# Optimization experiments

Hardware: AMD Instinct MI355X
Metric: run time of the kernel (lower is better)

## Reference

```python
import jax, jax.numpy as jnp
import numpy as np

B, N_PIC, C, H, W, P = 32, 4, 3, 224, 224, 16
HP = H // P  # 14
NP = HP * HP  # 196 patches
D = C * P * P  # 768 = hidden_size


def setup_inputs() -> dict:
    key = jax.random.key(0)
    ks = jax.random.split(key, 12)
    s = 0.02
    def lin(k, din, dout):
        kw, kb = jax.random.split(k)
        return (jax.random.normal(kw, (din, dout), jnp.float32) * s,
                jax.random.normal(kb, (dout,), jnp.float32) * s)
    W1, b1 = lin(ks[0], D, D)
    Wq, bq = lin(ks[1], D, D)
    Wk, bk = lin(ks[2], D, D)
    Wv, bv = lin(ks[3], D, D)
    Wo1, bo1 = lin(ks[4], D, D)
    Wo2, bo2 = lin(ks[5], D, D)
    x = jax.random.normal(ks[6], (B, N_PIC, C, H, W), jnp.float32)
    return {"x": x, "W1": W1, "b1": b1, "Wq": Wq, "bq": bq, "Wk": Wk,
            "bk": bk, "Wv": Wv, "bv": bv, "Wo1": Wo1, "bo1": bo1,
            "Wo2": Wo2, "bo2": bo2}


def reference(x, W1, b1, Wq, bq, Wk, bk, Wv, bv, Wo1, bo1, Wo2, bo2):
    b = x.shape[0]
    # patchify: matches torch unfold(3,P,P).unfold(4,P,P) + permute + view
    # -> [b, N, num_patches, C*P*P] with (C, ph, pw) ordering in last dim
    p = x.reshape(b, N_PIC, C, HP, P, HP, P)
    p = p.transpose(0, 1, 3, 5, 2, 4, 6).reshape(b, N_PIC, NP, D)
    h = p @ W1 + b1  # [b, N, S, D]
    # attention: query always from picture 0; key/value per picture (batched)
    Q = h[:, 0] @ Wq + bq          # [b, S, D]
    K = h @ Wk + bk                # [b, N, S, D]
    V = h @ Wv + bv                # [b, N, S, D]
    scale = 1.0 / jnp.sqrt(jnp.float32(D))
    scores = jnp.einsum('bsd,bnmd->bnsm', Q, K) * scale  # [b, N, S, S]
    attn = jax.nn.softmax(scores, axis=-1)
    wv = jnp.einsum('bnsm,bnmd->bnsd', attn, V)           # [b, N, S, D]
    out = jax.nn.relu(wv @ Wo1 + bo1) @ Wo2 + bo2
    return out
```

## Files before the change

kernel.cpp:

```cpp
#include <hip/hip_runtime.h>

typedef __bf16 bf16;
typedef __bf16 bf16x8 __attribute__((ext_vector_type(8)));
typedef float  f32x4  __attribute__((ext_vector_type(4)));


__global__ __launch_bounds__(256) void patchify_k(const float* __restrict__ x,
                                                  bf16* __restrict__ p) {
  int t = blockIdx.x * 256 + threadIdx.x;
  if (t >= 128 * 3 * 14 * 16 * 14) return;
  int j  = t % 14; t /= 14;
  int ph = t % 16; t /= 16;
  int i  = t % 14; t /= 14;
  int c  = t % 3;  t /= 3;
  int bn = t;
  const float* src = x + (((long long)(bn * 3 + c) * 224 + (i * 16 + ph)) * 224 + j * 16);
  bf16* dst = p + ((long long)(bn * 196 + (i * 14 + j)) * 768 + c * 256 + ph * 16);
  bf16 tmp[16];
  for (int k = 0; k < 16; k += 4) {
    float4 f = *(const float4*)(src + k);
    tmp[k + 0] = (bf16)f.x; tmp[k + 1] = (bf16)f.y;
    tmp[k + 2] = (bf16)f.z; tmp[k + 3] = (bf16)f.w;
  }
  *(bf16x8*)(dst)     = *(bf16x8*)&tmp[0];
  *(bf16x8*)(dst + 8) = *(bf16x8*)&tmp[8];
}

__global__ __launch_bounds__(256) void wtrans_k(const float* __restrict__ w0,
                                                const float* __restrict__ w1,
                                                const float* __restrict__ w2,
                                                const float* __restrict__ w3,
                                                const float* __restrict__ w4,
                                                const float* __restrict__ w5,
                                                bf16* __restrict__ out) {
  __shared__ float tile[32][33];
  const float* W;
  switch (blockIdx.z) {
    case 0: W = w0; break; case 1: W = w1; break; case 2: W = w2; break;
    case 3: W = w3; break; case 4: W = w4; break; default: W = w5; break;
  }
  bf16* o = out + (long long)blockIdx.z * 768 * 768;
  int nb = blockIdx.x * 32, kb = blockIdx.y * 32;
  int c = threadIdx.x & 31, r = threadIdx.x >> 5;
  for (int rr = 0; rr < 32; rr += 8)
    tile[r + rr][c] = W[(long long)(kb + r + rr) * 768 + nb + c];
  __syncthreads();
  for (int rr = 0; rr < 32; rr += 8)
    o[(long long)(nb + r + rr) * 768 + kb + c] = (bf16)tile[c][r + rr];
}

__global__ __launch_bounds__(256) void vtrans_k(const bf16* __restrict__ V,
                                                bf16* __restrict__ Vt) {
  __shared__ short tile[32][33];
  int z = blockIdx.z;
  const short* v = (const short*)(V + (long long)z * 196 * 768);
  short* vt = (short*)(Vt + (long long)z * 768 * 224);
  int db = blockIdx.x * 32;
  int mb = blockIdx.y * 32;
  int c = threadIdx.x & 31, r = threadIdx.x >> 5;
  for (int rr = 0; rr < 32; rr += 8) {
    int m = mb + r + rr;
    short val = 0;
    if (m < 196) val = v[(long long)m * 768 + db + c];
    tile[r + rr][c] = val;
  }
  __syncthreads();
  for (int rr = 0; rr < 32; rr += 8) {
    int d = db + r + rr;
    vt[(long long)d * 224 + mb + c] = tile[c][r + rr];
  }
}

__global__ __launch_bounds__(64) void softmax_k(const float* __restrict__ S,
                                                bf16* __restrict__ attn) {
  const int row = blockIdx.x;
  const float* sr = S + (long long)row * 196;
  const int l = threadIdx.x;
  float v0 = sr[l];
  float v1 = sr[l + 64];
  float v2 = sr[l + 128];
  float v3 = (l + 192 < 196) ? sr[l + 192] : -1e30f;
  float mx = fmaxf(fmaxf(v0, v1), fmaxf(v2, v3));
  for (int o = 32; o > 0; o >>= 1) mx = fmaxf(mx, __shfl_xor(mx, o));
  float e0 = __expf(v0 - mx);
  float e1 = __expf(v1 - mx);
  float e2 = __expf(v2 - mx);
  float e3 = (l + 192 < 196) ? __expf(v3 - mx) : 0.f;
  float s = e0 + e1 + e2 + e3;
  for (int o = 32; o > 0; o >>= 1) s += __shfl_xor(s, o);
  float inv = 1.0f / s;
  bf16* ar = attn + (long long)row * 224;
  ar[l]       = (bf16)(e0 * inv);
  ar[l + 64]  = (bf16)(e1 * inv);
  ar[l + 128] = (bf16)(e2 * inv);
  int m3 = l + 192;
  if (m3 < 196) ar[m3] = (bf16)(e3 * inv);
  else if (m3 < 224) ar[m3] = (bf16)0.0f;
}

__device__ __forceinline__ void gld16(const bf16* g, bf16* l) {
  __builtin_amdgcn_global_load_lds(
      (const __attribute__((address_space(1))) unsigned int*)g,
      (__attribute__((address_space(3))) unsigned int*)l, 16, 0, 0);
}

__global__ __launch_bounds__(256) void gemm128(
    const bf16* __restrict__ A, const bf16* __restrict__ Bt,
    const float* __restrict__ bias, void* __restrict__ Cout,
    int M, int N, int K, int gr, long long gs,
    long long strideAz, int a_zdiv, long long strideBz, long long strideCz,
    float scale, int relu, int out_bf16) {
  __shared__ __align__(16) bf16 As[128 * 32];
  __shared__ __align__(16) bf16 Bs[128 * 32];

  const int tid = threadIdx.x;
  const int lane = tid & 63;
  const int w = tid >> 6;
  const int wm = w & 1, wn = w >> 1;
  const int z = blockIdx.z;
  const int n0 = blockIdx.x * 128, m0 = blockIdx.y * 128;

  const bf16* Az  = A  + (long long)(z / a_zdiv) * strideAz;
  const bf16* Btz = Bt + (long long)z * strideBz;

  const int r0 = tid >> 2, kc0 = (tid & 3) * 8;
  int ar0 = m0 + r0;       if (ar0 >= M) ar0 = M - 1;
  int ar1 = m0 + 64 + r0;  if (ar1 >= M) ar1 = M - 1;
  const long long aoff0 = (long long)(ar0 / gr) * gs + (long long)(ar0 % gr) * K + kc0;
  const long long aoff1 = (long long)(ar1 / gr) * gs + (long long)(ar1 % gr) * K + kc0;
  int br0 = n0 + r0;       if (br0 >= N) br0 = N - 1;
  int br1 = n0 + 64 + r0;  if (br1 >= N) br1 = N - 1;
  const long long boff0 = (long long)br0 * K + kc0;
  const long long boff1 = (long long)br1 * K + kc0;

  bf16* asD0 = As + (long long)w * 512;
  bf16* asD1 = As + 2048 + (long long)w * 512;
  bf16* bsD0 = Bs + (long long)w * 512;
  bf16* bsD1 = Bs + 2048 + (long long)w * 512;

  f32x4 acc[4][4] = {};
  const int fr = lane & 15, fq = lane >> 4;

  for (int ko = 0; ko < K; ko += 32) {
    __syncthreads();
    gld16(Az + aoff0 + ko, asD0);
    gld16(Az + aoff1 + ko, asD1);
    gld16(Btz + boff0 + ko, bsD0);
    gld16(Btz + boff1 + ko, bsD1);
    __syncthreads();

    bf16x8 a[4], b[4];
#pragma unroll
    for (int mi = 0; mi < 4; mi++)
      a[mi] = *(const bf16x8*)&As[(wm * 64 + mi * 16 + fr) * 32 + fq * 8];
#pragma unroll
    for (int ni = 0; ni < 4; ni++)
      b[ni] = *(const bf16x8*)&Bs[(wn * 64 + ni * 16 + fr) * 32 + fq * 8];
#pragma unroll
    for (int mi = 0; mi < 4; mi++)
#pragma unroll
      for (int ni = 0; ni < 4; ni++)
        acc[mi][ni] = __builtin_amdgcn_mfma_f32_16x16x32_bf16(a[mi], b[ni], acc[mi][ni], 0, 0, 0);
  }

  const long long cz = (long long)z * strideCz;
#pragma unroll
  for (int ni = 0; ni < 4; ni++) {
    int col = n0 + wn * 64 + ni * 16 + fr;
    if (col >= N) continue;
    float bb = bias ? bias[col] : 0.f;
#pragma unroll
    for (int mi = 0; mi < 4; mi++) {
      int rbase = m0 + wm * 64 + mi * 16 + fq * 4;
#pragma unroll
      for (int r = 0; r < 4; r++) {
        int row = rbase + r;
        if (row >= M) continue;
        float v = acc[mi][ni][r] * scale + bb;
        if (relu) v = fmaxf(v, 0.f);
        long long idx = cz + (long long)row * N + col;
        if (out_bf16) ((bf16*)Cout)[idx] = (bf16)v;
        else          ((float*)Cout)[idx] = v;
      }
    }
  }
}

extern "C" void kernel_launch(void* const* d_in, const int* in_sizes, int n_in,
                              void* d_out, int out_size, void* d_ws, size_t ws_size,
                              hipStream_t stream) {
  (void)in_sizes; (void)n_in; (void)out_size; (void)ws_size;
  const float* x   = (const float*)d_in[0];
  const float* W1  = (const float*)d_in[1];
  const float* b1  = (const float*)d_in[2];
  const float* Wq  = (const float*)d_in[3];
  const float* bq  = (const float*)d_in[4];
  const float* Wk  = (const float*)d_in[5];
  const float* bk  = (const float*)d_in[6];
  const float* Wv  = (const float*)d_in[7];
  const float* bv  = (const float*)d_in[8];
  const float* Wo1 = (const float*)d_in[9];
  const float* bo1 = (const float*)d_in[10];
  const float* Wo2 = (const float*)d_in[11];
  const float* bo2 = (const float*)d_in[12];

  constexpr long long SZ_BIG = 25088LL * 768 * 2;
  char* ws = (char*)d_ws;
  bf16*  p    = (bf16*)(ws + 0);
  bf16*  h    = (bf16*)(ws + SZ_BIG);
  bf16*  q    = (bf16*)(ws + 2 * SZ_BIG);
  bf16*  kk   = (bf16*)(ws + 2 * SZ_BIG + 9633792LL);
  bf16*  vt   = (bf16*)(ws + 3 * SZ_BIG + 9633792LL);
  float* sc   = (float*)(ws + 3 * SZ_BIG + 9633792LL + 44040192LL);
  bf16*  attn = (bf16*)(ws + 3 * SZ_BIG + 9633792LL + 44040192LL + 19668992LL);
  bf16*  wt   = (bf16*)(ws + 3 * SZ_BIG + 9633792LL + 44040192LL + 19668992LL + 11239424LL);
  bf16*  v    = p;
  bf16*  wv   = h;
  bf16*  o1   = kk;
  constexpr long long WSZ = 768LL * 768;

  const float qk_scale = 0.03608439182435161f;

  patchify_k<<<4704, 256, 0, stream>>>(x, p);
  wtrans_k<<<dim3(24, 24, 6), 256, 0, stream>>>(W1, Wq, Wk, Wv, Wo1, Wo2, wt);

  gemm128<<<dim3(6, 196, 1), 256, 0, stream>>>(p, wt + 0 * WSZ, b1, h,
      25088, 768, 768, 25088, 0LL, 0LL, 1, 0LL, 0LL, 1.f, 0, 1);
  gemm128<<<dim3(6, 49, 1), 256, 0, stream>>>(h, wt + 1 * WSZ, bq, q,
      6272, 768, 768, 196, 602112LL, 0LL, 1, 0LL, 0LL, 1.f, 0, 1);
  gemm128<<<dim3(6, 196, 1), 256, 0, stream>>>(h, wt + 2 * WSZ, bk, kk,
      25088, 768, 768, 25088, 0LL, 0LL, 1, 0LL, 0LL, 1.f, 0, 1);
  gemm128<<<dim3(6, 196, 1), 256, 0, stream>>>(h, wt + 3 * WSZ, bv, v,
      25088, 768, 768, 25088, 0LL, 0LL, 1, 0LL, 0LL, 1.f, 0, 1);
  vtrans_k<<<dim3(24, 7, 128), 256, 0, stream>>>(v, vt);
  gemm128<<<dim3(2, 2, 128), 256, 0, stream>>>(q, kk, nullptr, sc,
      196, 196, 768, 196, 0LL, 150528LL, 4, 150528LL, 38416LL, qk_scale, 0, 0);
  softmax_k<<<25088, 64, 0, stream>>>(sc, attn);
  gemm128<<<dim3(6, 2, 128), 256, 0, stream>>>(attn, vt, nullptr, wv,
      196, 768, 224, 196, 0LL, 43904LL, 1, 172032LL, 150528LL, 1.f, 0, 1);
  gemm128<<<dim3(6, 196, 1), 256, 0, stream>>>(wv, wt + 4 * WSZ, bo1, o1,
      25088, 768, 768, 25088, 0LL, 0LL, 1, 0LL, 0LL, 1.f, 1, 1);
  gemm128<<<dim3(6, 196, 1), 256, 0, stream>>>(o1, wt + 5 * WSZ, bo2, (float*)d_out,
      25088, 768, 768, 25088, 0LL, 0LL, 1, 0LL, 0LL, 1.f, 0, 0);
}
```

Baseline: 688.1 us.

## Double-buffer GEMM LDS loads and fuse K/V projections into one GEMM

The GEMM kernel now double-buffers its LDS tiles. The next K-slice is issued with global_load_lds before the current slice's MFMAs run, and one barrier per iteration is dropped. The K and V projections are merged into a single N=1536 GEMM over the concatenated transposed weights, with split bias and lda/ldb parameters so the attention GEMMs and the V transpose can read the interleaved KV buffer. This reads h once for both projections and cuts a launch. In exchange it doubles LDS use per block and relies on a single barrier for correctness of the async LDS writes.

```diff
diff --git a/kernel.cpp b/kernel.cpp
--- a/kernel.cpp
+++ b/kernel.cpp
@@ -49,11 +49,11 @@
     o[(long long)(nb + r + rr) * 768 + kb + c] = (bf16)tile[c][r + rr];
 }
 
-__global__ __launch_bounds__(256) void vtrans_k(const bf16* __restrict__ V,
+__global__ __launch_bounds__(256) void vtrans_k(const bf16* __restrict__ kv,
                                                 bf16* __restrict__ Vt) {
   __shared__ short tile[32][33];
   int z = blockIdx.z;
-  const short* v = (const short*)(V + (long long)z * 196 * 768);
+  const short* v = (const short*)(kv + (long long)z * 301056 + 768);
   short* vt = (short*)(Vt + (long long)z * 768 * 224);
   int db = blockIdx.x * 32;
   int mb = blockIdx.y * 32;
@@ -61,7 +61,7 @@
   for (int rr = 0; rr < 32; rr += 8) {
     int m = mb + r + rr;
     short val = 0;
-    if (m < 196) val = v[(long long)m * 768 + db + c];
+    if (m < 196) val = v[(long long)m * 1536 + db + c];
     tile[r + rr][c] = val;
   }
   __syncthreads();
@@ -106,12 +106,13 @@
 
 __global__ __launch_bounds__(256) void gemm128(
     const bf16* __restrict__ A, const bf16* __restrict__ Bt,
-    const float* __restrict__ bias, void* __restrict__ Cout,
-    int M, int N, int K, int gr, long long gs,
+    const float* __restrict__ bias, const float* __restrict__ bias2,
+    void* __restrict__ Cout,
+    int M, int N, int K, int lda, int ldb, int gr, long long gs,
     long long strideAz, int a_zdiv, long long strideBz, long long strideCz,
     float scale, int relu, int out_bf16) {
-  __shared__ __align__(16) bf16 As[128 * 32];
-  __shared__ __align__(16) bf16 Bs[128 * 32];
+  __shared__ __align__(16) bf16 As[2][4096];
+  __shared__ __align__(16) bf16 Bs[2][4096];
 
   const int tid = threadIdx.x;
   const int lane = tid & 63;
@@ -126,36 +127,44 @@
   const int r0 = tid >> 2, kc0 = (tid & 3) * 8;
   int ar0 = m0 + r0;       if (ar0 >= M) ar0 = M - 1;
   int ar1 = m0 + 64 + r0;  if (ar1 >= M) ar1 = M - 1;
-  const long long aoff0 = (long long)(ar0 / gr) * gs + (long long)(ar0 % gr) * K + kc0;
-  const long long aoff1 = (long long)(ar1 / gr) * gs + (long long)(ar1 % gr) * K + kc0;
+  const bf16* aP0 = Az + (long long)(ar0 / gr) * gs + (long long)(ar0 % gr) * lda + kc0;
+  const bf16* aP1 = Az + (long long)(ar1 / gr) * gs + (long long)(ar1 % gr) * lda + kc0;
   int br0 = n0 + r0;       if (br0 >= N) br0 = N - 1;
   int br1 = n0 + 64 + r0;  if (br1 >= N) br1 = N - 1;
-  const long long boff0 = (long long)br0 * K + kc0;
-  const long long boff1 = (long long)br1 * K + kc0;
-
-  bf16* asD0 = As + (long long)w * 512;
-  bf16* asD1 = As + 2048 + (long long)w * 512;
-  bf16* bsD0 = Bs + (long long)w * 512;
-  bf16* bsD1 = Bs + 2048 + (long long)w * 512;
-
+  const bf16* bP0 = Btz + (long long)br0 * ldb + kc0;
+  const bf16* bP1 = Btz + (long long)br1 * ldb + kc0;
+
+  const int dstOff = w * 512;
+
+  const int niter = K >> 5;
   f32x4 acc[4][4] = {};
   const int fr = lane & 15, fq = lane >> 4;
 
-  for (int ko = 0; ko < K; ko += 32) {
+  gld16(aP0, As[0] + dstOff);
+  gld16(aP1, As[0] + 2048 + dstOff);
+  gld16(bP0, Bs[0] + dstOff);
+  gld16(bP1, Bs[0] + 2048 + dstOff);
+
+  for (int i = 0; i < niter; ++i) {
     __syncthreads();
-    gld16(Az + aoff0 + ko, asD0);
-    gld16(Az + aoff1 + ko, asD1);
-    gld16(Btz + boff0 + ko, bsD0);
-    gld16(Btz + boff1 + ko, bsD1);
-    __syncthreads();
-
+    const int cur = i & 1;
+    if (i + 1 < niter) {
+      const int nb = cur ^ 1;
+      const int off = (i + 1) << 5;
+      gld16(aP0 + off, As[nb] + dstOff);
+      gld16(aP1 + off, As[nb] + 2048 + dstOff);
+      gld16(bP0 + off, Bs[nb] + dstOff);
+      gld16(bP1 + off, Bs[nb] + 2048 + dstOff);
+    }
+    const bf16* Ac = As[cur];
+    const bf16* Bc = Bs[cur];
     bf16x8 a[4], b[4];
 #pragma unroll
     for (int mi = 0; mi < 4; mi++)
-      a[mi] = *(const bf16x8*)&As[(wm * 64 + mi * 16 + fr) * 32 + fq * 8];
+      a[mi] = *(const bf16x8*)&Ac[(wm * 64 + mi * 16 + fr) * 32 + fq * 8];
 #pragma unroll
     for (int ni = 0; ni < 4; ni++)
-      b[ni] = *(const bf16x8*)&Bs[(wn * 64 + ni * 16 + fr) * 32 + fq * 8];
+      b[ni] = *(const bf16x8*)&Bc[(wn * 64 + ni * 16 + fr) * 32 + fq * 8];
 #pragma unroll
     for (int mi = 0; mi < 4; mi++)
 #pragma unroll
@@ -168,7 +177,8 @@
   for (int ni = 0; ni < 4; ni++) {
     int col = n0 + wn * 64 + ni * 16 + fr;
     if (col >= N) continue;
-    float bb = bias ? bias[col] : 0.f;
+    float bb = 0.f;
+    if (bias) bb = (bias2 && col >= 768) ? bias2[col - 768] : bias[col];
 #pragma unroll
     for (int mi = 0; mi < 4; mi++) {
       int rbase = m0 + wm * 64 + mi * 16 + fq * 4;
@@ -204,42 +214,41 @@
   const float* Wo2 = (const float*)d_in[11];
   const float* bo2 = (const float*)d_in[12];
 
-  constexpr long long SZ_BIG = 25088LL * 768 * 2;
   char* ws = (char*)d_ws;
   bf16*  p    = (bf16*)(ws + 0);
-  bf16*  h    = (bf16*)(ws + SZ_BIG);
-  bf16*  q    = (bf16*)(ws + 2 * SZ_BIG);
-  bf16*  kk   = (bf16*)(ws + 2 * SZ_BIG + 9633792LL);
-  bf16*  vt   = (bf16*)(ws + 3 * SZ_BIG + 9633792LL);
-  float* sc   = (float*)(ws + 3 * SZ_BIG + 9633792LL + 44040192LL);
-  bf16*  attn = (bf16*)(ws + 3 * SZ_BIG + 9633792LL + 44040192LL + 19668992LL);
-  bf16*  wt   = (bf16*)(ws + 3 * SZ_BIG + 9633792LL + 44040192LL + 19668992LL + 11239424LL);
-  bf16*  v    = p;
-  bf16*  wv   = h;
-  bf16*  o1   = kk;
+  bf16*  vt   = (bf16*)(ws + 0);
+  bf16*  h    = (bf16*)(ws + 44040192LL);
+  bf16*  wv   = (bf16*)(ws + 44040192LL);
+  bf16*  kv   = (bf16*)(ws + 82575360LL);
+  bf16*  o1   = (bf16*)(ws + 82575360LL);
+  float* sc   = (float*)(ws + 159645696LL);
+  bf16*  q    = (bf16*)(ws + 179314688LL);
+  bf16*  attn = (bf16*)(ws + 179314688LL);
+  bf16*  wt   = (bf16*)(ws + 190554112LL);
   constexpr long long WSZ = 768LL * 768;
 
   const float qk_scale = 0.03608439182435161f;
 
   patchify_k<<<4704, 256, 0, stream>>>(x, p);
-  wtrans_k<<<dim3(24, 24, 6), 256, 0, stream>>>(W1, Wq, Wk, Wv, Wo1, Wo2, wt);
-
-  gemm128<<<dim3(6, 196, 1), 256, 0, stream>>>(p, wt + 0 * WSZ, b1, h,
-      25088, 768, 768, 25088, 0LL, 0LL, 1, 0LL, 0LL, 1.f, 0, 1);
-  gemm128<<<dim3(6, 49, 1), 256, 0, stream>>>(h, wt + 1 * WSZ, bq, q,
-      6272, 768, 768, 196, 602112LL, 0LL, 1, 0LL, 0LL, 1.f, 0, 1);
-  gemm128<<<dim3(6, 196, 1), 256, 0, stream>>>(h, wt + 2 * WSZ, bk, kk,
-      25088, 768, 768, 25088, 0LL, 0LL, 1, 0LL, 0LL, 1.f, 0, 1);
-  gemm128<<<dim3(6, 196, 1), 256, 0, stream>>>(h, wt + 3 * WSZ, bv, v,
-      25088, 768, 768, 25088, 0LL, 0LL, 1, 0LL, 0LL, 1.f, 0, 1);
-  vtrans_k<<<dim3(24, 7, 128), 256, 0, stream>>>(v, vt);
-  gemm128<<<dim3(2, 2, 128), 256, 0, stream>>>(q, kk, nullptr, sc,
-      196, 196, 768, 196, 0LL, 150528LL, 4, 150528LL, 38416LL, qk_scale, 0, 0);
+  wtrans_k<<<dim3(24, 24, 6), 256, 0, stream>>>(W1, Wk, Wv, Wq, Wo1, Wo2, wt);
+
+  gemm128<<<dim3(6, 196, 1), 256, 0, stream>>>(p, wt + 0 * WSZ, b1, nullptr, h,
+      25088, 768, 768, 768, 768, 25088, 0LL, 0LL, 1, 0LL, 0LL, 1.f, 0, 1);
+  gemm128<<<dim3(12, 196, 1), 256, 0, stream>>>(h, wt + 1 * WSZ, bk, bv, kv,
+      25088, 1536, 768, 768, 768, 25088, 0LL, 0LL, 1, 0LL, 0LL, 1.f, 0, 1);
+  gemm128<<<dim3(6, 49, 1), 256, 0, stream>>>(h, wt + 3 * WSZ, bq, nullptr, q,
+      6272, 768, 768, 768, 768, 196, 602112LL, 0LL, 1, 0LL, 0LL, 1.f, 0, 1);
+  vtrans_k<<<dim3(24, 7, 128), 256, 0, stream>>>(kv, vt);
+  gemm128<<<dim3(2, 2, 128), 256, 0, stream>>>(q, kv, nullptr, nullptr, sc,
+      196, 196, 768, 768, 1536, 196, 0LL, 150528LL, 4, 301056LL, 38416LL,
+      qk_scale, 0, 0);
   softmax_k<<<25088, 64, 0, stream>>>(sc, attn);
-  gemm128<<<dim3(6, 2, 128), 256, 0, stream>>>(attn, vt, nullptr, wv,
-      196, 768, 224, 196, 0LL, 43904LL, 1, 172032LL, 150528LL, 1.f, 0, 1);
-  gemm128<<<dim3(6, 196, 1), 256, 0, stream>>>(wv, wt + 4 * WSZ, bo1, o1,
-      25088, 768, 768, 25088, 0LL, 0LL, 1, 0LL, 0LL, 1.f, 1, 1);
-  gemm128<<<dim3(6, 196, 1), 256, 0, stream>>>(o1, wt + 5 * WSZ, bo2, (float*)d_out,
-      25088, 768, 768, 25088, 0LL, 0LL, 1, 0LL, 0LL, 1.f, 0, 0);
-}
+  gemm128<<<dim3(6, 2, 128), 256, 0, stream>>>(attn, vt, nullptr, nullptr, wv,
+      196, 768, 224, 224, 224, 196, 0LL, 43904LL, 1, 172032LL, 150528LL,
+      1.f, 0, 1);
+  gemm128<<<dim3(6, 196, 1), 256, 0, stream>>>(wv, wt + 4 * WSZ, bo1, nullptr, o1,
+      25088, 768, 768, 768, 768, 25088, 0LL, 0LL, 1, 0LL, 0LL, 1.f, 1, 1);
+  gemm128<<<dim3(6, 196, 1), 256, 0, stream>>>(o1, wt + 5 * WSZ, bo2, nullptr,
+      (float*)d_out,
+      25088, 768, 768, 768, 768, 25088, 0LL, 0LL, 1, 0LL, 0LL, 1.f, 0, 0);
+}
```

After: 646.8 us. 1.06x faster.
